# Kernel tuning notes

Measured on AMD Instinct MI355X. Metric: run time of the kernel, lower is better.

The kernel has to match this reference:

```python
import jax, jax.numpy as jnp
import numpy as np
import itertools

# 3x3x3 neighborhood geometry: 27 cells, offsets in itertools.product order,
# so index 13 is the center voxel.
_POS = np.array(list(itertools.product([-1, 0, 1], repeat=3)))  # [27,3]
_DIFF = _POS[:, None, :] - _POS[None, :, :]
_A18 = (np.abs(_DIFF).sum(-1) <= 2)   # 18-connectivity (scipy structure s in source)
_A26 = (np.abs(_DIFF).max(-1) <= 1)   # 26-connectivity (np.ones((3,3,3)))
_CENTER = 13


def _cc_label_6(fg):
    """Connected-component labels of 3D bool array under 6-connectivity
    (scipy.ndimage.label default structure). Background = 0; each component
    gets a distinct positive id (min linear index + 1) via min-propagation."""
    n = fg.size
    BIG = jnp.int32(n + 2)
    idx = jnp.arange(1, n + 1, dtype=jnp.int32).reshape(fg.shape)
    lab0 = jnp.where(fg, idx, BIG)

    def step(lab):
        p = jnp.pad(lab, 1, mode='constant', constant_values=n + 2)
        m = lab
        m = jnp.minimum(m, p[:-2, 1:-1, 1:-1])
        m = jnp.minimum(m, p[2:, 1:-1, 1:-1])
        m = jnp.minimum(m, p[1:-1, :-2, 1:-1])
        m = jnp.minimum(m, p[1:-1, 2:, 1:-1])
        m = jnp.minimum(m, p[1:-1, 1:-1, :-2])
        m = jnp.minimum(m, p[1:-1, 1:-1, 2:])
        return jnp.where(fg, m, BIG)

    def cond(c):
        return c[1]

    def body(c):
        lab = c[0]
        new = step(lab)
        return (new, jnp.any(new != lab))

    lab, _ = jax.lax.while_loop(cond, body, (lab0, jnp.array(True)))
    return jnp.where(fg, lab, 0)


def _count_components(mask, adj_np):
    """mask: [V,27] bool. Counts connected components of the True cells in each
    27-cell neighborhood under adjacency adj_np (matches scipy label num_features).
    Min-label propagation for 26 steps (>= max path length in a 27-node graph)."""
    BIG = jnp.int32(27)
    ids = jnp.arange(27, dtype=jnp.int32)
    adj = jnp.asarray(adj_np)
    init = jnp.where(mask, ids[None, :], BIG)

    def body(_, lab):
        new = lab
        for j in range(27):
            contrib = jnp.where(mask[:, j], lab[:, j], BIG)[:, None]  # [V,1]
            new = jnp.minimum(new, jnp.where(adj[:, j][None, :], contrib, BIG))
        return jnp.where(mask, new, BIG)

    lab = jax.lax.fori_loop(0, 26, body, init)
    # a component's root keeps its own index -> count roots
    return jnp.sum(mask & (lab == ids[None, :]), axis=1)  # [V]


def _nonsimple_points(x, threshold=0.5):
    """JAX version of label_nonsimple_points: 1.0 where voxel is a non-simple
    point of the thresholded volume, else 0.0."""
    D, H, W = x.shape
    fg = x > threshold
    lab = _cc_label_6(fg)                       # [D,H,W] int32, 0 = background
    p = jnp.pad(lab, 1, mode='edge')            # np.pad(..., 'edge') in source
    nb = jnp.stack(
        [p[dz + 1:dz + 1 + D, dy + 1:dy + 1 + H, dx + 1:dx + 1 + W]
         for dz, dy, dx in _POS], axis=-1).reshape(-1, 27)  # [V,27]
    center = nb[:, _CENTER]
    # Test 1: cells differing from the center's component id (incl. background),
    # 18-connectivity; simple requires exactly one component.
    c1 = _count_components(nb != center[:, None], _A18)
    # Test 2: cells equal to the center's component, center removed,
    # 26-connectivity; simple requires exactly one component.
    m2 = (nb == center[:, None]).at[:, _CENTER].set(False)
    c2 = _count_components(m2, _A26)
    ns = (center != 0) & ((c1 != 1) | (c2 != 1))
    return ns.reshape(x.shape).astype(x.dtype)


def _weight_tensor(x, simple_weight=1.0, non_simple_weight=10.0):
    ns = jax.lax.stop_gradient(_nonsimple_points(x))
    w = simple_weight * (1.0 - ns) + non_simple_weight * ns
    return w * x


def setup_inputs() -> dict:
    key = jax.random.key(0)
    k1, k2 = jax.random.split(key)
    pred = jax.random.normal(k1, (64, 64, 64), dtype=jnp.float32)
    target = jax.random.uniform(k2, (64, 64, 64), dtype=jnp.float32)
    return {"pred": pred, "target": target}


def reference(pred, target):
    wp = _weight_tensor(pred)
    wl = _weight_tensor(target)
    # err = -(wl * -log(1+e^{-wp}) + (1-wl) * -log(1+e^{wp}))
    err = wl * jax.nn.softplus(-wp) + (1.0 - wl) * jax.nn.softplus(wp)
    return jnp.sum(err)
```

## Files before the change

### kernel.cpp

```cpp
#include <hip/hip_runtime.h>

#define NINV 0xFFFFFFFFu
static constexpr int D = 64, H = 64, W = 64;
static constexpr int NVOX = D * H * W;
static constexpr int NTOT = 2 * NVOX;


__device__ __forceinline__ unsigned find_c(unsigned* P, unsigned i) {
    unsigned p = P[i];
    while (p != i) {
        unsigned gp = P[p];
        if (gp == p) return p;
        P[i] = gp;
        i = gp;
        p = P[i];
    }
    return i;
}

__device__ void unite(unsigned* P, unsigned a, unsigned b) {
    for (;;) {
        a = find_c(P, a);
        b = find_c(P, b);
        if (a == b) return;
        if (a > b) { unsigned t = a; a = b; b = t; }
        unsigned old = atomicCAS(&P[b], b, a);
        if (old == b || old == a) return;
        b = old;
    }
}


__global__ __launch_bounds__(512) void local_ccl_k(const float* __restrict__ pred,
                                                   const float* __restrict__ target,
                                                   unsigned* __restrict__ parent) {
    __shared__ unsigned lab[512];
    int tb  = blockIdx.x & 511;
    int vol = blockIdx.x >> 9;
    const float* src = vol ? target : pred;
    int tx = (tb & 7) << 3;
    int ty = ((tb >> 3) & 7) << 3;
    int tz = (tb >> 6) << 3;

    int l = threadIdx.x;
    int lx = l & 7, ly = (l >> 3) & 7, lz = l >> 6;
    int g = ((tz + lz) << 12) + ((ty + ly) << 6) + (tx + lx);

    bool fg = src[g] > 0.5f;
    lab[l] = fg ? (unsigned)l : NINV;
    __syncthreads();

    for (;;) {
        int my_changed = 0;
        if (fg) {
            unsigned cur = lab[l];
            unsigned m = cur;
            if (lx > 0) m = min(m, lab[l - 1]);
            if (lx < 7) m = min(m, lab[l + 1]);
            if (ly > 0) m = min(m, lab[l - 8]);
            if (ly < 7) m = min(m, lab[l + 8]);
            if (lz > 0) m = min(m, lab[l - 64]);
            if (lz < 7) m = min(m, lab[l + 64]);
            for (;;) { unsigned p = lab[m]; if (p >= m) break; m = p; }
            if (m < cur) { lab[l] = m; my_changed = 1; }
        }
        if (__syncthreads_count(my_changed) == 0) break;
    }

    unsigned r = NINV;
    if (fg) {
        unsigned rr = lab[l];
        r = (unsigned)(vol * NVOX)
          + (unsigned)(((tz + (int)(rr >> 6)) << 12)
                     + ((ty + (int)((rr >> 3) & 7)) << 6)
                     +  (tx + (int)(rr & 7)));
    }
    parent[vol * NVOX + g] = r;
}


static constexpr int FACES_PER_DIR = 7 * 8 * 8;
static constexpr int FACES_PER_VOL = 3 * FACES_PER_DIR;
static constexpr int FACES_TOT     = 2 * FACES_PER_VOL;

__global__ void merge_k(unsigned* __restrict__ parent) {
    int wave = (int)((blockIdx.x * blockDim.x + threadIdx.x) >> 6);
    int lane = threadIdx.x & 63;
    if (wave >= FACES_TOT) return;
    int vol = wave / FACES_PER_VOL;
    int f   = wave - vol * FACES_PER_VOL;
    int dir = f / FACES_PER_DIR;
    int ff  = f - dir * FACES_PER_DIR;
    int plane = ff >> 6;
    int tf    = ff & 63;
    int a0 = ((tf & 7) << 3) + (lane & 7);
    int a1 = ((tf >> 3) << 3) + (lane >> 3);
    int x, y, z, stride;
    if (dir == 0)      { x = plane * 8 + 7; y = a0; z = a1; stride = 1; }
    else if (dir == 1) { y = plane * 8 + 7; x = a0; z = a1; stride = 64; }
    else               { z = plane * 8 + 7; x = a0; y = a1; stride = 4096; }
    int i = vol * NVOX + (z << 12) + (y << 6) + x;

    unsigned ra = parent[i];
    unsigned rb = parent[i + stride];
    bool valid = (ra != NINV) && (rb != NINV);
    unsigned long long key = valid ? (((unsigned long long)ra << 32) | rb) : ~0ull;

    bool leader = valid;
    #pragma unroll 8
    for (int j = 0; j < 64; ++j) {
        unsigned long long kj = __shfl(key, j, 64);
        if (j < lane && kj == key) leader = false;
    }
    if (leader) unite(parent, ra, rb);
}


static constexpr unsigned ALL27 = 0x7FFFFFFu;
static constexpr unsigned XL2 = 0x36DB6DBu;
static constexpr unsigned XG0 = 0x6DB6DB6u;
static constexpr unsigned YL2 = 0x0FC7E3Fu;
static constexpr unsigned YG0 = 0x7E3F1F8u;
static constexpr unsigned ZL2 = 0x003FFFFu;
static constexpr unsigned ZG0 = 0x7FFFE00u;
static constexpr unsigned X0  = 0x1249249u;
static constexpr unsigned X2  = 0x4924924u;
static constexpr unsigned Y0  = 0x01C0E07u;
static constexpr unsigned Y2  = 0x70381C0u;
static constexpr unsigned Z0  = 0x00001FFu;
static constexpr unsigned Z2  = 0x7FC0000u;

__device__ __forceinline__ unsigned dilX(unsigned m) {
    return m | ((m & XL2) << 1) | ((m & XG0) >> 1);
}
__device__ __forceinline__ unsigned dilY(unsigned m) {
    return m | ((m & YL2) << 3) | ((m & YG0) >> 3);
}
__device__ __forceinline__ unsigned dilZ(unsigned m) {
    return m | ((m & ZL2) << 9) | ((m & ZG0) >> 9);
}
__device__ __forceinline__ unsigned dil2(unsigned m) {
    return ((m & X0) << 2) | ((m & X2) >> 2)
         | ((m & Y0) << 6) | ((m & Y2) >> 6)
         | ((m & Z0) << 18) | ((m & Z2) >> 18);
}

__device__ __forceinline__ bool multi18(unsigned mask) {
    if (mask == 0) return true;
    unsigned comp = mask & (0u - mask);
    for (;;) {
        unsigned a = dilX(comp), b = dilY(comp);
        unsigned n = (dilY(a) | dilZ(a) | dilZ(b) | dil2(comp)) & mask;
        if (n == comp) break;
        comp = n;
    }
    return comp != mask;
}

__device__ __forceinline__ bool multi26(unsigned mask) {
    if (mask == 0) return true;
    unsigned comp = mask & (0u - mask);
    for (;;) {
        unsigned n = dilZ(dilY(dilX(comp))) & mask;
        if (n == comp) break;
        comp = n;
    }
    return comp != mask;
}

__device__ __forceinline__ float weight_lds(const unsigned* __restrict__ h,
                                            int lx, int ly, int lz) {
    int ctr = (lz + 1) * 100 + (ly + 1) * 10 + (lx + 1);
    unsigned c = h[ctr];
    if (c == NINV) return 1.0f;
    unsigned same = 0;
    int k = 0;
    #pragma unroll
    for (int dz = 0; dz <= 2; ++dz) {
        #pragma unroll
        for (int dy = 0; dy <= 2; ++dy) {
            int base = (lz + dz) * 100 + (ly + dy) * 10 + lx;
            #pragma unroll
            for (int dx = 0; dx <= 2; ++dx) {
                same |= (h[base + dx] == c ? 1u : 0u) << k;
                ++k;
            }
        }
    }
    unsigned m1 = (~same) & ALL27;
    unsigned m2 = same & ~(1u << 13);
    bool ns = multi18(m1) || multi26(m2);
    return ns ? 10.0f : 1.0f;
}

__global__ __launch_bounds__(512) void final_k(const float* __restrict__ pred,
                                               const float* __restrict__ target,
                                               unsigned* __restrict__ parent,
                                               float* __restrict__ out) {
    __shared__ unsigned hP[1000], hT[1000];
    __shared__ float sred[8];

    int l = threadIdx.x;
    int tb = blockIdx.x;
    int tx = (tb & 7) << 3;
    int ty = ((tb >> 3) & 7) << 3;
    int tz = (tb >> 6) << 3;

    for (int e = l; e < 1000; e += 512) {
        int hx = e % 10, hy = (e / 10) % 10, hz = e / 100;
        int gx = min(max(tx + hx - 1, 0), 63);
        int gy = min(max(ty + hy - 1, 0), 63);
        int gz = min(max(tz + hz - 1, 0), 63);
        int g = (gz << 12) + (gy << 6) + gx;
        unsigned p = parent[g];
        if (p != NINV) { unsigned q; while ((q = parent[p]) != p) p = q; }
        hP[e] = p;
        unsigned s = parent[NVOX + g];
        if (s != NINV) { unsigned q; while ((q = parent[s]) != s) s = q; }
        hT[e] = s;
    }
    __syncthreads();

    int lx = l & 7, ly = (l >> 3) & 7, lz = l >> 6;
    int g = ((tz + lz) << 12) + ((ty + ly) << 6) + (tx + lx);

    float wP = weight_lds(hP, lx, ly, lz);
    float wT = weight_lds(hT, lx, ly, lz);
    float wp = wP * pred[g];
    float wl = wT * target[g];
    float l1pe = log1pf(expf(-fabsf(wp)));
    float sp_pos = fmaxf(wp, 0.0f) + l1pe;
    float sp_neg = fmaxf(-wp, 0.0f) + l1pe;
    float err = wl * sp_neg + (1.0f - wl) * sp_pos;

    #pragma unroll
    for (int o = 32; o > 0; o >>= 1) err += __shfl_down(err, o, 64);
    int lane = l & 63;
    int wv = l >> 6;
    if (lane == 0) sred[wv] = err;
    __syncthreads();
    if (l == 0) {
        float s = 0.0f;
        #pragma unroll
        for (int w = 0; w < 8; ++w) s += sred[w];
        atomicAdd(out, s);
    }
}


extern "C" void kernel_launch(void* const* d_in, const int* in_sizes, int n_in,
                              void* d_out, int out_size, void* d_ws, size_t ws_size,
                              hipStream_t stream) {
    const float* pred   = (const float*)d_in[0];
    const float* target = (const float*)d_in[1];
    float* out = (float*)d_out;
    unsigned* parent = (unsigned*)d_ws;

    hipMemsetAsync(d_out, 0, sizeof(float), stream);

    local_ccl_k<<<1024, 512, 0, stream>>>(pred, target, parent);
    merge_k<<<FACES_TOT * 64 / 256, 256, 0, stream>>>(parent);
    final_k<<<512, 512, 0, stream>>>(pred, target, parent, out);
}
```

Before: 111.0 us.

## Fuse CCL, merge and final stages into one cooperative kernel with grid syncs

```diff
diff --git a/kernel.cpp b/kernel.cpp
--- a/kernel.cpp
+++ b/kernel.cpp
@@ -1,4 +1,7 @@
 #include <hip/hip_runtime.h>
+#include <hip/hip_cooperative_groups.h>
+
+namespace cg = cooperative_groups;
 
 #define NINV 0xFFFFFFFFu
 static constexpr int D = 64, H = 64, W = 64;
@@ -31,114 +34,17 @@
 }
 
 
-__global__ __launch_bounds__(512) void local_ccl_k(const float* __restrict__ pred,
-                                                   const float* __restrict__ target,
-                                                   unsigned* __restrict__ parent) {
-    __shared__ unsigned lab[512];
-    int tb  = blockIdx.x & 511;
-    int vol = blockIdx.x >> 9;
-    const float* src = vol ? target : pred;
-    int tx = (tb & 7) << 3;
-    int ty = ((tb >> 3) & 7) << 3;
-    int tz = (tb >> 6) << 3;
-
-    int l = threadIdx.x;
-    int lx = l & 7, ly = (l >> 3) & 7, lz = l >> 6;
-    int g = ((tz + lz) << 12) + ((ty + ly) << 6) + (tx + lx);
-
-    bool fg = src[g] > 0.5f;
-    lab[l] = fg ? (unsigned)l : NINV;
-    __syncthreads();
-
-    for (;;) {
-        int my_changed = 0;
-        if (fg) {
-            unsigned cur = lab[l];
-            unsigned m = cur;
-            if (lx > 0) m = min(m, lab[l - 1]);
-            if (lx < 7) m = min(m, lab[l + 1]);
-            if (ly > 0) m = min(m, lab[l - 8]);
-            if (ly < 7) m = min(m, lab[l + 8]);
-            if (lz > 0) m = min(m, lab[l - 64]);
-            if (lz < 7) m = min(m, lab[l + 64]);
-            for (;;) { unsigned p = lab[m]; if (p >= m) break; m = p; }
-            if (m < cur) { lab[l] = m; my_changed = 1; }
-        }
-        if (__syncthreads_count(my_changed) == 0) break;
-    }
-
-    unsigned r = NINV;
-    if (fg) {
-        unsigned rr = lab[l];
-        r = (unsigned)(vol * NVOX)
-          + (unsigned)(((tz + (int)(rr >> 6)) << 12)
-                     + ((ty + (int)((rr >> 3) & 7)) << 6)
-                     +  (tx + (int)(rr & 7)));
-    }
-    parent[vol * NVOX + g] = r;
-}
-
-
-static constexpr int FACES_PER_DIR = 7 * 8 * 8;
-static constexpr int FACES_PER_VOL = 3 * FACES_PER_DIR;
-static constexpr int FACES_TOT     = 2 * FACES_PER_VOL;
-
-__global__ void merge_k(unsigned* __restrict__ parent) {
-    int wave = (int)((blockIdx.x * blockDim.x + threadIdx.x) >> 6);
-    int lane = threadIdx.x & 63;
-    if (wave >= FACES_TOT) return;
-    int vol = wave / FACES_PER_VOL;
-    int f   = wave - vol * FACES_PER_VOL;
-    int dir = f / FACES_PER_DIR;
-    int ff  = f - dir * FACES_PER_DIR;
-    int plane = ff >> 6;
-    int tf    = ff & 63;
-    int a0 = ((tf & 7) << 3) + (lane & 7);
-    int a1 = ((tf >> 3) << 3) + (lane >> 3);
-    int x, y, z, stride;
-    if (dir == 0)      { x = plane * 8 + 7; y = a0; z = a1; stride = 1; }
-    else if (dir == 1) { y = plane * 8 + 7; x = a0; z = a1; stride = 64; }
-    else               { z = plane * 8 + 7; x = a0; y = a1; stride = 4096; }
-    int i = vol * NVOX + (z << 12) + (y << 6) + x;
-
-    unsigned ra = parent[i];
-    unsigned rb = parent[i + stride];
-    bool valid = (ra != NINV) && (rb != NINV);
-    unsigned long long key = valid ? (((unsigned long long)ra << 32) | rb) : ~0ull;
-
-    bool leader = valid;
-    #pragma unroll 8
-    for (int j = 0; j < 64; ++j) {
-        unsigned long long kj = __shfl(key, j, 64);
-        if (j < lane && kj == key) leader = false;
-    }
-    if (leader) unite(parent, ra, rb);
-}
-
-
 static constexpr unsigned ALL27 = 0x7FFFFFFu;
-static constexpr unsigned XL2 = 0x36DB6DBu;
-static constexpr unsigned XG0 = 0x6DB6DB6u;
-static constexpr unsigned YL2 = 0x0FC7E3Fu;
-static constexpr unsigned YG0 = 0x7E3F1F8u;
-static constexpr unsigned ZL2 = 0x003FFFFu;
-static constexpr unsigned ZG0 = 0x7FFFE00u;
-static constexpr unsigned X0  = 0x1249249u;
-static constexpr unsigned X2  = 0x4924924u;
-static constexpr unsigned Y0  = 0x01C0E07u;
-static constexpr unsigned Y2  = 0x70381C0u;
-static constexpr unsigned Z0  = 0x00001FFu;
-static constexpr unsigned Z2  = 0x7FC0000u;
-
-__device__ __forceinline__ unsigned dilX(unsigned m) {
-    return m | ((m & XL2) << 1) | ((m & XG0) >> 1);
-}
-__device__ __forceinline__ unsigned dilY(unsigned m) {
-    return m | ((m & YL2) << 3) | ((m & YG0) >> 3);
-}
-__device__ __forceinline__ unsigned dilZ(unsigned m) {
-    return m | ((m & ZL2) << 9) | ((m & ZG0) >> 9);
-}
+static constexpr unsigned XL2 = 0x36DB6DBu, XG0 = 0x6DB6DB6u;
+static constexpr unsigned YL2 = 0x0FC7E3Fu, YG0 = 0x7E3F1F8u;
+static constexpr unsigned ZL2 = 0x003FFFFu, ZG0 = 0x7FFFE00u;
+static constexpr unsigned X0 = 0x1249249u, X2 = 0x4924924u;
+static constexpr unsigned Y0 = 0x01C0E07u, Y2 = 0x70381C0u;
+static constexpr unsigned Z0 = 0x00001FFu, Z2 = 0x7FC0000u;
+
+__device__ __forceinline__ unsigned dilX(unsigned m) { return m | ((m & XL2) << 1) | ((m & XG0) >> 1); }
+__device__ __forceinline__ unsigned dilY(unsigned m) { return m | ((m & YL2) << 3) | ((m & YG0) >> 3); }
+__device__ __forceinline__ unsigned dilZ(unsigned m) { return m | ((m & ZL2) << 9) | ((m & ZG0) >> 9); }
 __device__ __forceinline__ unsigned dil2(unsigned m) {
     return ((m & X0) << 2) | ((m & X2) >> 2)
          | ((m & Y0) << 6) | ((m & Y2) >> 6)
@@ -189,40 +95,137 @@
     }
     unsigned m1 = (~same) & ALL27;
     unsigned m2 = same & ~(1u << 13);
-    bool ns = multi18(m1) || multi26(m2);
-    return ns ? 10.0f : 1.0f;
-}
-
-__global__ __launch_bounds__(512) void final_k(const float* __restrict__ pred,
-                                               const float* __restrict__ target,
-                                               unsigned* __restrict__ parent,
-                                               float* __restrict__ out) {
-    __shared__ unsigned hP[1000], hT[1000];
+    return (multi18(m1) || multi26(m2)) ? 10.0f : 1.0f;
+}
+
+
+static constexpr int FACES_PER_DIR = 7 * 8 * 8;
+static constexpr int FACES_PER_VOL = 3 * FACES_PER_DIR;
+static constexpr int FACES_TOT     = 2 * FACES_PER_VOL;
+
+
+__global__ __launch_bounds__(512, 4) void fused_k(const float* __restrict__ pred,
+                                                  const float* __restrict__ target,
+                                                  unsigned* __restrict__ parent,
+                                                  float* __restrict__ out) {
+    cg::grid_group grid = cg::this_grid();
+    __shared__ unsigned sh[2000];
     __shared__ float sred[8];
 
-    int l = threadIdx.x;
     int tb = blockIdx.x;
+    int l  = threadIdx.x;
     int tx = (tb & 7) << 3;
     int ty = ((tb >> 3) & 7) << 3;
     int tz = (tb >> 6) << 3;
-
+    int lx = l & 7, ly = (l >> 3) & 7, lz = l >> 6;
+    int g = ((tz + lz) << 12) + ((ty + ly) << 6) + (tx + lx);
+
+    unsigned* lab0 = sh;
+    unsigned* lab1 = sh + 512;
+    bool fg0 = pred[g]   > 0.5f;
+    bool fg1 = target[g] > 0.5f;
+    lab0[l] = fg0 ? (unsigned)l : NINV;
+    lab1[l] = fg1 ? (unsigned)l : NINV;
+    __syncthreads();
+
+    for (;;) {
+        int ch = 0;
+        if (fg0) {
+            unsigned cur = lab0[l], m = cur;
+            if (lx > 0) m = min(m, lab0[l - 1]);
+            if (lx < 7) m = min(m, lab0[l + 1]);
+            if (ly > 0) m = min(m, lab0[l - 8]);
+            if (ly < 7) m = min(m, lab0[l + 8]);
+            if (lz > 0) m = min(m, lab0[l - 64]);
+            if (lz < 7) m = min(m, lab0[l + 64]);
+            for (;;) { unsigned p = lab0[m]; if (p >= m) break; m = p; }
+            if (m < cur) { lab0[l] = m; ch = 1; }
+        }
+        if (fg1) {
+            unsigned cur = lab1[l], m = cur;
+            if (lx > 0) m = min(m, lab1[l - 1]);
+            if (lx < 7) m = min(m, lab1[l + 1]);
+            if (ly > 0) m = min(m, lab1[l - 8]);
+            if (ly < 7) m = min(m, lab1[l + 8]);
+            if (lz > 0) m = min(m, lab1[l - 64]);
+            if (lz < 7) m = min(m, lab1[l + 64]);
+            for (;;) { unsigned p = lab1[m]; if (p >= m) break; m = p; }
+            if (m < cur) { lab1[l] = m; ch = 1; }
+        }
+        if (__syncthreads_count(ch) == 0) break;
+    }
+
+    unsigned r0 = NINV, r1 = NINV;
+    if (fg0) {
+        unsigned rr = lab0[l];
+        r0 = (unsigned)(((tz + (int)(rr >> 6)) << 12)
+                      + ((ty + (int)((rr >> 3) & 7)) << 6)
+                      +  (tx + (int)(rr & 7)));
+    }
+    if (fg1) {
+        unsigned rr = lab1[l];
+        r1 = (unsigned)NVOX
+           + (unsigned)(((tz + (int)(rr >> 6)) << 12)
+                      + ((ty + (int)((rr >> 3) & 7)) << 6)
+                      +  (tx + (int)(rr & 7)));
+    }
+    parent[g] = r0;
+    parent[NVOX + g] = r1;
+    if (tb == 0 && l == 0) atomicExch(out, 0.0f);
+
+    grid.sync();
+
+    {
+        int wave = tb * 8 + (l >> 6);
+        int lane = l & 63;
+        if (wave < FACES_TOT) {
+            int vol = wave / FACES_PER_VOL;
+            int f   = wave - vol * FACES_PER_VOL;
+            int dir = f / FACES_PER_DIR;
+            int ff  = f - dir * FACES_PER_DIR;
+            int plane = ff >> 6;
+            int tf    = ff & 63;
+            int a0 = ((tf & 7) << 3) + (lane & 7);
+            int a1 = ((tf >> 3) << 3) + (lane >> 3);
+            int x, y, z, stride;
+            if (dir == 0)      { x = plane * 8 + 7; y = a0; z = a1; stride = 1; }
+            else if (dir == 1) { y = plane * 8 + 7; x = a0; z = a1; stride = 64; }
+            else               { z = plane * 8 + 7; x = a0; y = a1; stride = 4096; }
+            int i = vol * NVOX + (z << 12) + (y << 6) + x;
+
+            unsigned ra = parent[i];
+            unsigned rb = parent[i + stride];
+            bool valid = (ra != NINV) && (rb != NINV);
+            unsigned long long key = valid ? (((unsigned long long)ra << 32) | rb) : ~0ull;
+
+            bool leader = valid;
+            #pragma unroll 8
+            for (int j = 0; j < 64; ++j) {
+                unsigned long long kj = __shfl(key, j, 64);
+                if (j < lane && kj == key) leader = false;
+            }
+            if (leader) unite(parent, ra, rb);
+        }
+    }
+
+    grid.sync();
+
+    unsigned* hP = sh;
+    unsigned* hT = sh + 1000;
     for (int e = l; e < 1000; e += 512) {
         int hx = e % 10, hy = (e / 10) % 10, hz = e / 100;
         int gx = min(max(tx + hx - 1, 0), 63);
         int gy = min(max(ty + hy - 1, 0), 63);
         int gz = min(max(tz + hz - 1, 0), 63);
-        int g = (gz << 12) + (gy << 6) + gx;
-        unsigned p = parent[g];
+        int gg = (gz << 12) + (gy << 6) + gx;
+        unsigned p = parent[gg];
         if (p != NINV) { unsigned q; while ((q = parent[p]) != p) p = q; }
         hP[e] = p;
-        unsigned s = parent[NVOX + g];
+        unsigned s = parent[NVOX + gg];
         if (s != NINV) { unsigned q; while ((q = parent[s]) != s) s = q; }
         hT[e] = s;
     }
     __syncthreads();
-
-    int lx = l & 7, ly = (l >> 3) & 7, lz = l >> 6;
-    int g = ((tz + lz) << 12) + ((ty + ly) << 6) + (tx + lx);
 
     float wP = weight_lds(hP, lx, ly, lz);
     float wT = weight_lds(hT, lx, ly, lz);
@@ -256,9 +259,7 @@
     float* out = (float*)d_out;
     unsigned* parent = (unsigned*)d_ws;
 
-    hipMemsetAsync(d_out, 0, sizeof(float), stream);
-
-    local_ccl_k<<<1024, 512, 0, stream>>>(pred, target, parent);
-    merge_k<<<FACES_TOT * 64 / 256, 256, 0, stream>>>(parent);
-    final_k<<<512, 512, 0, stream>>>(pred, target, parent, out);
-}
+    void* args[] = { (void*)&pred, (void*)&target, (void*)&parent, (void*)&out };
+    hipLaunchCooperativeKernel((const void*)fused_k, dim3(512), dim3(512),
+                               args, 0, stream);
+}
```

Result: slower. 220.4 us (+98.5%).
